# Kernel optimization log

Measured on AMD Instinct MI355X. Metric: run time of the kernel, lower is better.

Reference implementation:

```python
import jax, jax.numpy as jnp
import numpy as np

D_QUERY = 512
D_AUDIO = 512
D_OUT = 512
B, HW, S = 16, 4096, 1024


def setup_inputs() -> dict:
    key = jax.random.key(0)
    ks = jax.random.split(key, 8)
    sc_q = 1.0 / np.sqrt(D_QUERY)
    sc_a = 1.0 / np.sqrt(D_AUDIO)
    return {
        "x": jax.random.normal(ks[0], (B, HW, D_QUERY), dtype=jnp.float32),
        "audio_embed": jax.random.normal(ks[1], (B, S, D_AUDIO), dtype=jnp.float32),
        "Wq": jax.random.uniform(ks[2], (D_QUERY, D_OUT), jnp.float32, -sc_q, sc_q),
        "bq": jax.random.uniform(ks[3], (D_OUT,), jnp.float32, -sc_q, sc_q),
        "Wk": jax.random.uniform(ks[4], (D_AUDIO, D_OUT), jnp.float32, -sc_a, sc_a),
        "bk": jax.random.uniform(ks[5], (D_OUT,), jnp.float32, -sc_a, sc_a),
        "Wv": jax.random.uniform(ks[6], (D_AUDIO, D_OUT), jnp.float32, -sc_a, sc_a),
        "bv": jax.random.uniform(ks[7], (D_OUT,), jnp.float32, -sc_a, sc_a),
    }


def reference(x, audio_embed, Wq, bq, Wk, bk, Wv, bv):
    # Linear projections (nn.Linear: y = x @ W^T + b; we store W already transposed)
    Q = x @ Wq + bq                      # [B, HW, D_OUT]
    K = audio_embed @ Wk + bk            # [B, S, D_OUT]
    V = audio_embed @ Wv + bv            # [B, S, D_OUT]
    scale = 1.0 / (K.shape[-1] ** 0.5)   # divide by sqrt(d_out), per source
    scores = jnp.einsum("bnd,bsd->bns", Q, K) * scale  # [B, HW, S]
    attn = jax.nn.softmax(scores, axis=-1)
    return jnp.einsum("bns,bsd->bnd", attn, V)         # [B, HW, D_OUT]
```

## Files before the change

### kernel.cpp

```cpp
#include <hip/hip_runtime.h>
#include <hip/hip_bf16.h>

typedef __attribute__((ext_vector_type(8))) short bf16x8;
typedef __attribute__((ext_vector_type(4))) float f32x4;
typedef __attribute__((ext_vector_type(4))) unsigned short ushort4v;

#define AS1 __attribute__((address_space(1)))
#define AS3 __attribute__((address_space(3)))

__device__ __forceinline__ float bf_bits_to_f(short s) {
  unsigned int u = ((unsigned int)(unsigned short)s) << 16;
  union { unsigned int u; float f; } c; c.u = u; return c.f;
}
__device__ __forceinline__ unsigned short f_to_bf_bits(float f) {
  union { float f; unsigned int u; } c; c.f = f;
  unsigned int r = c.u + 0x7FFFu + ((c.u >> 16) & 1u);
  return (unsigned short)(r >> 16);
}

__device__ __forceinline__ int fsw(int row) { return ((row >> 1) & 3) << 4; }

__global__ __launch_bounds__(256) void cvt_bf16_kernel(const float* __restrict__ in,
                                                       unsigned short* __restrict__ out,
                                                       long n) {
  const long nchunks = n >> 2;
  const long stride = (long)gridDim.x * 256;
  for (long c = (long)blockIdx.x * 256 + threadIdx.x; c < nchunks; c += stride) {
    f32x4 v = *(const f32x4*)(in + c * 4);
    ushort4v o;
    o[0] = f_to_bf_bits(v[0]); o[1] = f_to_bf_bits(v[1]);
    o[2] = f_to_bf_bits(v[2]); o[3] = f_to_bf_bits(v[3]);
    *(ushort4v*)(out + c * 4) = o;
  }
}

__global__ __launch_bounds__(256) void transpose1_kernel(
    const float* __restrict__ W, unsigned short* __restrict__ T) {
  __shared__ float t[32][33];
  const int tx = threadIdx.x & 31, ty = threadIdx.x >> 5;
  const int n0 = blockIdx.x * 32, k0 = blockIdx.y * 32;
#pragma unroll
  for (int j = 0; j < 4; ++j)
    t[ty + 8 * j][tx] = W[(long)(k0 + ty + 8 * j) * 512 + n0 + tx];
  __syncthreads();
#pragma unroll
  for (int j = 0; j < 4; ++j)
    T[(long)(n0 + ty + 8 * j) * 512 + k0 + tx] = f_to_bf_bits(t[tx][ty + 8 * j]);
}

__global__ __launch_bounds__(256) void wvec_kernel(const float* __restrict__ Wk,
                                                   const float* __restrict__ bq,
                                                   float* __restrict__ w, const float s) {
  const int q = blockIdx.x * 4 + (threadIdx.x >> 6);
  const int lane = threadIdx.x & 63;
  const float* row = Wk + (long)q * 512 + lane * 8;
  const f32x4 a0 = *(const f32x4*)row;
  const f32x4 a1 = *(const f32x4*)(row + 4);
  const f32x4 b0 = *(const f32x4*)(bq + lane * 8);
  const f32x4 b1 = *(const f32x4*)(bq + lane * 8 + 4);
  float d = a0[0]*b0[0] + a0[1]*b0[1] + a0[2]*b0[2] + a0[3]*b0[3]
          + a1[0]*b1[0] + a1[1]*b1[1] + a1[2]*b1[2] + a1[3]*b1[3];
  for (int off = 1; off < 64; off <<= 1) d += __shfl_xor(d, off);
  if (lane == 0) w[q] = d * s;
}

__global__ __launch_bounds__(256) void cvec_kernel(const unsigned short* __restrict__ ab,
                                                   const float* __restrict__ w,
                                                   float* __restrict__ cv) {
  const long row = (long)blockIdx.x * 4 + (threadIdx.x >> 6);
  const int lane = threadIdx.x & 63;
  const bf16x8 a = *(const bf16x8*)(ab + row * 512 + lane * 8);
  const f32x4 w0 = *(const f32x4*)(w + lane * 8);
  const f32x4 w1 = *(const f32x4*)(w + lane * 8 + 4);
  float d = 0.f;
#pragma unroll
  for (int e = 0; e < 4; ++e) d += bf_bits_to_f(a[e]) * w0[e];
#pragma unroll
  for (int e = 0; e < 4; ++e) d += bf_bits_to_f(a[4 + e]) * w1[e];
  for (int off = 1; off < 64; off <<= 1) d += __shfl_xor(d, off);
  if (lane == 0) cv[row] = d;
}

template <bool BIAS, bool TRANSOUT, bool AFP32>
__global__ __launch_bounds__(256) void gemm_kernel(
    const void* __restrict__ Aptr,
    const unsigned short* __restrict__ BT,
    const float* __restrict__ bias,
    unsigned short* __restrict__ Cout,
    const int K, const float scale,
    const long strideA, const long strideBT, const long strideC, const int ldc,
    const int nx, const int ny) {
  __shared__ unsigned short lds[8192];
  const int nwg = gridDim.x;
  const int chunk = nwg >> 3;
  const int bid = blockIdx.x;
  const int swz = (bid & 7) * chunk + (bid >> 3);
  const int bx = swz % nx;
  const int t1 = swz / nx;
  const int by = t1 % ny;
  const int bz = t1 / ny;

  const int tid = threadIdx.x;
  const int lane = tid & 63;
  const int wv = tid >> 6;
  const int wr = wv >> 1, wc = wv & 1;
  const unsigned short* Ab = (const unsigned short*)Aptr + (long)bz * strideA + (long)by * 128 * K;
  const float* Af = (const float*)Aptr + (long)bz * strideA + (long)by * 128 * K;
  const unsigned short* Bb = BT + (long)bz * strideBT + (long)bx * 128 * K;

  f32x4 acc[4][4];
#pragma unroll
  for (int m = 0; m < 4; ++m)
#pragma unroll
    for (int n = 0; n < 4; ++n) acc[m][n] = (f32x4){0.f, 0.f, 0.f, 0.f};

  const int r15 = lane & 15, g = lane >> 4;
  const int kiters = K >> 5;
  const int asw = fsw(r15);

  int arow[2], acs[2];
#pragma unroll
  for (int i = 0; i < 2; ++i) {
    const int c = i * 4 + wv;
    const int boff = c * 1024 + lane * 16;
    arow[i] = boff >> 6;
    acs[i] = (boff & 63) ^ fsw(arow[i]);
  }
  f32x4 pa[2][2];
  if (AFP32) {
#pragma unroll
    for (int i = 0; i < 2; ++i) {
      const float* s = Af + (long)arow[i] * K + (acs[i] >> 1);
      pa[i][0] = *(const f32x4*)s;
      pa[i][1] = *(const f32x4*)(s + 4);
    }
  }

  for (int kt = 0; kt < kiters; ++kt) {
#pragma unroll
    for (int i = 0; i < 2; ++i) {
      const int c = i * 4 + wv;
      const char* srcB = (const char*)Bb + (long)arow[i] * (K * 2) + kt * 64 + acs[i];
      __builtin_amdgcn_global_load_lds(
          (const AS1 void*)srcB, (AS3 void*)(lds + 4096 + c * 512), 16, 0, 0);
      if (!AFP32) {
        const char* srcA = (const char*)Ab + (long)arow[i] * (K * 2) + kt * 64 + acs[i];
        __builtin_amdgcn_global_load_lds(
            (const AS1 void*)srcA, (AS3 void*)(lds + c * 512), 16, 0, 0);
      }
    }
    if (AFP32) {
#pragma unroll
      for (int i = 0; i < 2; ++i) {
        const int c = i * 4 + wv;
        bf16x8 w;
#pragma unroll
        for (int e = 0; e < 4; ++e) {
          w[e] = (short)f_to_bf_bits(pa[i][0][e]);
          w[4 + e] = (short)f_to_bf_bits(pa[i][1][e]);
        }
        *(bf16x8*)&lds[c * 512 + lane * 8] = w;
      }
      if (kt < kiters - 1) {
#pragma unroll
        for (int i = 0; i < 2; ++i) {
          const float* s = Af + (long)arow[i] * K + (kt + 1) * 32 + (acs[i] >> 1);
          pa[i][0] = *(const f32x4*)s;
          pa[i][1] = *(const f32x4*)(s + 4);
        }
      }
    }
    __syncthreads();

    bf16x8 af[4], bf[4];
#pragma unroll
    for (int m = 0; m < 4; ++m)
      af[m] = *(const bf16x8*)((const char*)lds + (wr * 64 + m * 16 + r15) * 64 + (g * 16 ^ asw));
#pragma unroll
    for (int n = 0; n < 4; ++n)
      bf[n] = *(const bf16x8*)((const char*)lds + 8192 +
                               (wc * 64 + n * 16 + r15) * 64 + (g * 16 ^ asw));
#pragma unroll
    for (int m = 0; m < 4; ++m)
#pragma unroll
      for (int n = 0; n < 4; ++n)
        acc[m][n] = __builtin_amdgcn_mfma_f32_16x16x32_bf16(af[m], bf[n], acc[m][n], 0, 0, 0);
    __syncthreads();
  }

  const long crow0 = (long)by * 128 + wr * 64;
  const long ccol0 = (long)bx * 128 + wc * 64;
#pragma unroll
  for (int n = 0; n < 4; ++n) {
    const long col = ccol0 + n * 16 + r15;
    const float bv = BIAS ? bias[col] : 0.f;
#pragma unroll
    for (int m = 0; m < 4; ++m) {
      const f32x4 v = acc[m][n];
#pragma unroll
      for (int j = 0; j < 4; ++j) {
        const long row = crow0 + m * 16 + g * 4 + j;
        const float val = (v[j] + bv) * scale;
        const long idx = TRANSOUT ? (col * (long)ldc + row) : (row * (long)ldc + col);
        (Cout + (long)bz * strideC)[idx] = f_to_bf_bits(val);
      }
    }
  }
}

template <bool EXPSTATS, bool DIVSTATS>
__global__ __launch_bounds__(512, 2) void gemm256_kernel(
    const unsigned short* __restrict__ A,
    const unsigned short* __restrict__ BT,
    void* __restrict__ Cout,
    const int K,
    const long strideA, const long strideBT, const long strideC, const int ldc,
    const int nx, const int ny, float* __restrict__ stats,
    const float* __restrict__ cbias) {
  __shared__ __align__(16) char halfb[4][32768];
  __shared__ float ssum[256][4];
  __shared__ float invl[256];

  const int nwg = gridDim.x;
  const int chunk = nwg >> 3;
  const int bid = blockIdx.x;
  const int swz = (bid & 7) * chunk + (bid >> 3);
  const int bx = swz % nx;
  const int t1 = swz / nx;
  const int by = t1 % ny;
  const int bz = t1 / ny;

  const int tid = threadIdx.x;
  const int lane = tid & 63;
  const int w = tid >> 6;
  const int wm = w >> 2, wn = w & 3;
  const int r15 = lane & 15, g = lane >> 4;
  const int asw = fsw(r15);

  const char* Abyt = (const char*)(A + (long)bz * strideA + (long)by * 256 * K);
  const char* Bbyt = (const char*)(BT + (long)bz * strideBT + (long)bx * 256 * K);
  const long rsb = (long)K * 2;

  if (DIVSTATS) {
    if (tid < 256) {
      const f32x4 s = *(const f32x4*)&stats[((long)bz * 4096 + (long)by * 256 + tid) * 4];
      invl[tid] = 1.f / (s[0] + s[1] + s[2] + s[3]);
    }
  }
  __builtin_amdgcn_sched_barrier(0);

  const int srow0 = tid >> 2;
  const int scol = ((tid & 3) << 4) ^ fsw(srow0);
  const long aoff0 = (long)srow0 * rsb + scol;
  const long aoff1 = (long)(srow0 + 128) * rsb + scol;
  const int dbase = tid * 16;

  auto stage = [&](int s) {
    char* h = halfb[s & 3];
    const long kb = (long)s * 64;
    __builtin_amdgcn_global_load_lds((const AS1 void*)(Abyt + aoff0 + kb),
                                     (AS3 void*)(h + dbase), 16, 0, 0);
    __builtin_amdgcn_global_load_lds((const AS1 void*)(Abyt + aoff1 + kb),
                                     (AS3 void*)(h + 8192 + dbase), 16, 0, 0);
    __builtin_amdgcn_global_load_lds((const AS1 void*)(Bbyt + aoff0 + kb),
                                     (AS3 void*)(h + 16384 + dbase), 16, 0, 0);
    __builtin_amdgcn_global_load_lds((const AS1 void*)(Bbyt + aoff1 + kb),
                                     (AS3 void*)(h + 24576 + dbase), 16, 0, 0);
  };

  f32x4 acc[8][4];
#pragma unroll
  for (int m = 0; m < 8; ++m)
#pragma unroll
    for (int n = 0; n < 4; ++n) acc[m][n] = (f32x4){0.f, 0.f, 0.f, 0.f};

  const int kslices = K >> 5;

  stage(0);
  stage(1);
  stage(2);
  asm volatile("s_waitcnt vmcnt(8)" ::: "memory");
  __builtin_amdgcn_s_barrier();
  __builtin_amdgcn_sched_barrier(0);

  for (int s = 0; s < kslices; ++s) {
    const char* hA = halfb[s & 3];
    const char* hB = halfb[s & 3] + 16384;
    bf16x8 fa[8], fb[4];
#pragma unroll
    for (int m = 0; m < 8; ++m)
      fa[m] = *(const bf16x8*)(hA + (wm * 128 + m * 16 + r15) * 64 + ((g * 16) ^ asw));
#pragma unroll
    for (int n = 0; n < 4; ++n)
      fb[n] = *(const bf16x8*)(hB + (wn * 64 + n * 16 + r15) * 64 + ((g * 16) ^ asw));
    __builtin_amdgcn_sched_barrier(0);
    if (s < kslices - 2) asm volatile("s_waitcnt vmcnt(4)" ::: "memory");
    else                 asm volatile("s_waitcnt vmcnt(0)" ::: "memory");
    __builtin_amdgcn_s_barrier();
    asm volatile("s_waitcnt lgkmcnt(0)" ::: "memory");
    __builtin_amdgcn_sched_barrier(0);
    if (s + 3 < kslices) stage(s + 3);
    __builtin_amdgcn_s_setprio(1);
#pragma unroll
    for (int m = 0; m < 8; ++m)
#pragma unroll
      for (int n = 0; n < 4; ++n)
        acc[m][n] = __builtin_amdgcn_mfma_f32_16x16x32_bf16(fa[m], fb[n], acc[m][n], 0, 0, 0);
    __builtin_amdgcn_s_setprio(0);
    __builtin_amdgcn_sched_barrier(0);
  }

  if (EXPSTATS) {
    float cb[4];
#pragma unroll
    for (int n = 0; n < 4; ++n)
      cb[n] = cbias[(long)bz * 1024 + (long)bx * 256 + wn * 64 + n * 16 + r15];
#pragma unroll
    for (int m = 0; m < 8; ++m)
#pragma unroll
      for (int n = 0; n < 4; ++n)
#pragma unroll
        for (int j = 0; j < 4; ++j) acc[m][n][j] = __expf(acc[m][n][j] + cb[n]);
#pragma unroll
    for (int m = 0; m < 8; ++m)
#pragma unroll
      for (int j = 0; j < 4; ++j) {
        float s = acc[m][0][j] + acc[m][1][j] + acc[m][2][j] + acc[m][3][j];
        s += __shfl_xor(s, 1);
        s += __shfl_xor(s, 2);
        s += __shfl_xor(s, 4);
        s += __shfl_xor(s, 8);
        if (r15 == 0) ssum[wm * 128 + m * 16 + g * 4 + j][wn] = s;
      }
    __syncthreads();
    if (tid < 256) {
      const float t = ssum[tid][0] + ssum[tid][1] + ssum[tid][2] + ssum[tid][3];
      stats[((long)bz * 4096 + (long)by * 256 + tid) * 4 + bx] = t;
    }
  }

  const long crow0 = (long)by * 256 + wm * 128;
  const long ccol0 = (long)bx * 256 + wn * 64;
#pragma unroll
  for (int m = 0; m < 8; ++m)
#pragma unroll
    for (int j = 0; j < 4; ++j) {
      const int rl = wm * 128 + m * 16 + g * 4 + j;
      const long row = crow0 + m * 16 + g * 4 + j;
#pragma unroll
      for (int n = 0; n < 4; ++n) {
        const long col = ccol0 + n * 16 + r15;
        if (EXPSTATS) {
          ((unsigned short*)Cout + (long)bz * strideC)[row * (long)ldc + col] =
              f_to_bf_bits(acc[m][n][j]);
        } else {
          const float sc = DIVSTATS ? invl[rl] : 1.f;
          ((float*)Cout + (long)bz * strideC)[row * (long)ldc + col] = acc[m][n][j] * sc;
        }
      }
    }
}

extern "C" void kernel_launch(void* const* d_in, const int* in_sizes, int n_in,
                              void* d_out, int out_size, void* d_ws, size_t ws_size,
                              hipStream_t stream) {
  (void)in_sizes; (void)n_in; (void)out_size; (void)ws_size;
  const float* x     = (const float*)d_in[0];
  const float* audio = (const float*)d_in[1];
  const float* Wq    = (const float*)d_in[2];
  const float* bq    = (const float*)d_in[3];
  const float* Wk    = (const float*)d_in[4];
  const float* bk    = (const float*)d_in[5];  (void)bk;
  const float* Wv    = (const float*)d_in[6];
  const float* bv    = (const float*)d_in[7];
  float* out = (float*)d_out;

  const float s = 0.044194173824159216f;

  char* ws = (char*)d_ws;
  size_t off = 0;
  auto carve = [&](size_t bytes) { char* p = ws + off; off += (bytes + 255) & ~(size_t)255; return p; };
  unsigned short* xb  = (unsigned short*)carve((size_t)65536 * 512 * 2);
  unsigned short* ab  = (unsigned short*)carve((size_t)16384 * 512 * 2);
  unsigned short* wkb = (unsigned short*)carve((size_t)512 * 512 * 2);
  unsigned short* wvt = (unsigned short*)carve((size_t)512 * 512 * 2);
  unsigned short* G   = (unsigned short*)carve((size_t)512 * 512 * 2);
  unsigned short* KMb = (unsigned short*)carve((size_t)16384 * 512 * 2);
  unsigned short* Vt  = (unsigned short*)carve((size_t)16384 * 512 * 2);
  unsigned short* Pb  = (unsigned short*)carve((size_t)65536 * 1024 * 2);
  float*          ls  = (float*)carve((size_t)65536 * 4 * 4);
  float*          wv_ = (float*)carve((size_t)512 * 4);
  float*          cv  = (float*)carve((size_t)16384 * 4);

  cvt_bf16_kernel<<<2048, 256, 0, stream>>>(x, xb, (long)65536 * 512);
  cvt_bf16_kernel<<<1024, 256, 0, stream>>>(audio, ab, (long)16384 * 512);
  cvt_bf16_kernel<<<256, 256, 0, stream>>>(Wk, wkb, (long)512 * 512);
  transpose1_kernel<<<dim3(16, 16), 256, 0, stream>>>(Wv, wvt);
  gemm_kernel<false, false, true><<<16, 256, 0, stream>>>(
      Wq, wkb, nullptr, G, 512, s, 0, 0, 0, 512, 4, 4);
  wvec_kernel<<<128, 256, 0, stream>>>(Wk, bq, wv_, s);
  cvec_kernel<<<4096, 256, 0, stream>>>(ab, wv_, cv);
  gemm_kernel<true, true, false><<<4 * 8 * 16, 256, 0, stream>>>(
      ab, wvt, bv, Vt, 512, 1.f, (long)1024 * 512, 0, (long)512 * 1024, 1024, 4, 8);
  gemm_kernel<false, false, false><<<4 * 8 * 16, 256, 0, stream>>>(
      ab, G, nullptr, KMb, 512, 1.f, (long)1024 * 512, 0, (long)1024 * 512, 512, 4, 8);
  gemm256_kernel<true, false><<<4 * 16 * 16, 512, 0, stream>>>(
      xb, KMb, Pb, 512,
      (long)4096 * 512, (long)1024 * 512, (long)4096 * 1024, 1024, 4, 16, ls, cv);
  gemm256_kernel<false, true><<<2 * 16 * 16, 512, 0, stream>>>(
      Pb, Vt, out, 1024,
      (long)4096 * 1024, (long)512 * 1024, (long)4096 * 512, 512, 2, 16, ls, nullptr);
}
```

Baseline: 328.5 us.

## Fuse fp32-to-bf16 conversion into GEMM loaders and merge V/K projections

```diff
diff --git a/kernel.cpp b/kernel.cpp
--- a/kernel.cpp
+++ b/kernel.cpp
@@ -64,19 +64,17 @@
   if (lane == 0) w[q] = d * s;
 }
 
-__global__ __launch_bounds__(256) void cvec_kernel(const unsigned short* __restrict__ ab,
+__global__ __launch_bounds__(256) void cvec_kernel(const float* __restrict__ audio,
                                                    const float* __restrict__ w,
                                                    float* __restrict__ cv) {
   const long row = (long)blockIdx.x * 4 + (threadIdx.x >> 6);
   const int lane = threadIdx.x & 63;
-  const bf16x8 a = *(const bf16x8*)(ab + row * 512 + lane * 8);
+  const f32x4 a0 = *(const f32x4*)(audio + row * 512 + lane * 8);
+  const f32x4 a1 = *(const f32x4*)(audio + row * 512 + lane * 8 + 4);
   const f32x4 w0 = *(const f32x4*)(w + lane * 8);
   const f32x4 w1 = *(const f32x4*)(w + lane * 8 + 4);
-  float d = 0.f;
-#pragma unroll
-  for (int e = 0; e < 4; ++e) d += bf_bits_to_f(a[e]) * w0[e];
-#pragma unroll
-  for (int e = 0; e < 4; ++e) d += bf_bits_to_f(a[4 + e]) * w1[e];
+  float d = a0[0]*w0[0] + a0[1]*w0[1] + a0[2]*w0[2] + a0[3]*w0[3]
+          + a1[0]*w1[0] + a1[1]*w1[1] + a1[2]*w1[2] + a1[3]*w1[3];
   for (int off = 1; off < 64; off <<= 1) d += __shfl_xor(d, off);
   if (lane == 0) cv[row] = d;
 }
@@ -208,9 +206,126 @@
   }
 }
 
-template <bool EXPSTATS, bool DIVSTATS>
+__global__ __launch_bounds__(256) void projdual_kernel(
+    const float* __restrict__ audio,
+    const unsigned short* __restrict__ wvt,
+    const unsigned short* __restrict__ G,
+    const float* __restrict__ bv,
+    unsigned short* __restrict__ Vt,
+    unsigned short* __restrict__ KMb) {
+  __shared__ unsigned short lds[8192];
+  const int nwg = gridDim.x;
+  const int chunk = nwg >> 3;
+  const int bid = blockIdx.x;
+  const int swz = (bid & 7) * chunk + (bid >> 3);
+  const int bx = swz & 7;
+  const int t1 = swz >> 3;
+  const int by = t1 & 7;
+  const int bz = t1 >> 3;
+
+  const int tid = threadIdx.x;
+  const int lane = tid & 63;
+  const int wv = tid >> 6;
+  const int wr = wv >> 1, wc = wv & 1;
+  const float* Af = audio + (long)bz * 1024 * 512 + (long)by * 128 * 512;
+  const unsigned short* Bb = (bx < 4) ? (wvt + (long)bx * 128 * 512)
+                                      : (G + (long)(bx - 4) * 128 * 512);
+
+  f32x4 acc[4][4];
+#pragma unroll
+  for (int m = 0; m < 4; ++m)
+#pragma unroll
+    for (int n = 0; n < 4; ++n) acc[m][n] = (f32x4){0.f, 0.f, 0.f, 0.f};
+
+  const int r15 = lane & 15, g = lane >> 4;
+  const int asw = fsw(r15);
+
+  int arow[2], acs[2];
+#pragma unroll
+  for (int i = 0; i < 2; ++i) {
+    const int c = i * 4 + wv;
+    const int boff = c * 1024 + lane * 16;
+    arow[i] = boff >> 6;
+    acs[i] = (boff & 63) ^ fsw(arow[i]);
+  }
+  f32x4 pa[2][2];
+#pragma unroll
+  for (int i = 0; i < 2; ++i) {
+    const float* s = Af + (long)arow[i] * 512 + (acs[i] >> 1);
+    pa[i][0] = *(const f32x4*)s;
+    pa[i][1] = *(const f32x4*)(s + 4);
+  }
+
+  for (int kt = 0; kt < 16; ++kt) {
+#pragma unroll
+    for (int i = 0; i < 2; ++i) {
+      const int c = i * 4 + wv;
+      const char* srcB = (const char*)Bb + (long)arow[i] * 1024 + kt * 64 + acs[i];
+      __builtin_amdgcn_global_load_lds(
+          (const AS1 void*)srcB, (AS3 void*)(lds + 4096 + c * 512), 16, 0, 0);
+    }
+#pragma unroll
+    for (int i = 0; i < 2; ++i) {
+      const int c = i * 4 + wv;
+      bf16x8 w;
+#pragma unroll
+      for (int e = 0; e < 4; ++e) {
+        w[e] = (short)f_to_bf_bits(pa[i][0][e]);
+        w[4 + e] = (short)f_to_bf_bits(pa[i][1][e]);
+      }
+      *(bf16x8*)&lds[c * 512 + lane * 8] = w;
+    }
+    if (kt < 15) {
+#pragma unroll
+      for (int i = 0; i < 2; ++i) {
+        const float* s = Af + (long)arow[i] * 512 + (kt + 1) * 32 + (acs[i] >> 1);
+        pa[i][0] = *(const f32x4*)s;
+        pa[i][1] = *(const f32x4*)(s + 4);
+      }
+    }
+    __syncthreads();
+
+    bf16x8 af[4], bf[4];
+#pragma unroll
+    for (int m = 0; m < 4; ++m)
+      af[m] = *(const bf16x8*)((const char*)lds + (wr * 64 + m * 16 + r15) * 64 + (g * 16 ^ asw));
+#pragma unroll
+    for (int n = 0; n < 4; ++n)
+      bf[n] = *(const bf16x8*)((const char*)lds + 8192 +
+                               (wc * 64 + n * 16 + r15) * 64 + (g * 16 ^ asw));
+#pragma unroll
+    for (int m = 0; m < 4; ++m)
+#pragma unroll
+      for (int n = 0; n < 4; ++n)
+        acc[m][n] = __builtin_amdgcn_mfma_f32_16x16x32_bf16(af[m], bf[n], acc[m][n], 0, 0, 0);
+    __syncthreads();
+  }
+
+  const long crow0 = (long)by * 128 + wr * 64;
+  const long ccol0 = (long)bx * 128 + wc * 64;
+#pragma unroll
+  for (int n = 0; n < 4; ++n) {
+    const long col = ccol0 + n * 16 + r15;
+    const float bvv = (bx < 4) ? bv[col] : 0.f;
+#pragma unroll
+    for (int m = 0; m < 4; ++m) {
+      const f32x4 v = acc[m][n];
+#pragma unroll
+      for (int j = 0; j < 4; ++j) {
+        const long row = crow0 + m * 16 + g * 4 + j;
+        const float val = v[j] + bvv;
+        if (bx < 4)
+          Vt[(long)bz * 512 * 1024 + col * 1024 + row] = f_to_bf_bits(val);
+        else
+          KMb[(long)bz * 1024 * 512 + row * 512 + (col - 512)] = f_to_bf_bits(val);
+      }
+    }
+  }
+}
+
+template <bool EXPSTATS, bool DIVSTATS, bool AFP32>
 __global__ __launch_bounds__(512, 2) void gemm256_kernel(
-    const unsigned short* __restrict__ A,
+    const void* __restrict__ Aptr,
     const unsigned short* __restrict__ BT,
     void* __restrict__ Cout,
     const int K,
@@ -237,7 +352,9 @@
   const int r15 = lane & 15, g = lane >> 4;
   const int asw = fsw(r15);
 
-  const char* Abyt = (const char*)(A + (long)bz * strideA + (long)by * 256 * K);
+  const unsigned short* Abf = (const unsigned short*)Aptr + (long)bz * strideA + (long)by * 256 * K;
+  const float* Afp = (const float*)Aptr + (long)bz * strideA + (long)by * 256 * K;
+  const char* Abyt = (const char*)Abf;
   const char* Bbyt = (const char*)(BT + (long)bz * strideBT + (long)bx * 256 * K);
   const long rsb = (long)K * 2;
 
@@ -254,19 +371,26 @@
   const long aoff0 = (long)srow0 * rsb + scol;
   const long aoff1 = (long)(srow0 + 128) * rsb + scol;
   const int dbase = tid * 16;
-
+  const float* AF0 = Afp + (long)srow0 * K + (scol >> 1);
+  const float* AF1 = Afp + (long)(srow0 + 128) * K + (scol >> 1);
+
+  auto gl = [&](const char* src, char* dst) {
+    __builtin_amdgcn_global_load_lds((const AS1 void*)src, (AS3 void*)dst, 16, 0, 0);
+  };
   auto stage = [&](int s) {
     char* h = halfb[s & 3];
     const long kb = (long)s * 64;
-    __builtin_amdgcn_global_load_lds((const AS1 void*)(Abyt + aoff0 + kb),
-                                     (AS3 void*)(h + dbase), 16, 0, 0);
-    __builtin_amdgcn_global_load_lds((const AS1 void*)(Abyt + aoff1 + kb),
-                                     (AS3 void*)(h + 8192 + dbase), 16, 0, 0);
-    __builtin_amdgcn_global_load_lds((const AS1 void*)(Bbyt + aoff0 + kb),
-                                     (AS3 void*)(h + 16384 + dbase), 16, 0, 0);
-    __builtin_amdgcn_global_load_lds((const AS1 void*)(Bbyt + aoff1 + kb),
-                                     (AS3 void*)(h + 24576 + dbase), 16, 0, 0);
+    gl(Abyt + aoff0 + kb, h + dbase);
+    gl(Abyt + aoff1 + kb, h + 8192 + dbase);
+    gl(Bbyt + aoff0 + kb, h + 16384 + dbase);
+    gl(Bbyt + aoff1 + kb, h + 24576 + dbase);
   };
+  auto stageB = [&](int s) {
+    char* h = halfb[s & 3];
+    const long kb = (long)s * 64;
+    gl(Bbyt + aoff0 + kb, h + 16384 + dbase);
+    gl(Bbyt + aoff1 + kb, h + 24576 + dbase);
+  };
 
   f32x4 acc[8][4];
 #pragma unroll
@@ -275,40 +399,98 @@
     for (int n = 0; n < 4; ++n) acc[m][n] = (f32x4){0.f, 0.f, 0.f, 0.f};
 
   const int kslices = K >> 5;
-
-  stage(0);
-  stage(1);
-  stage(2);
-  asm volatile("s_waitcnt vmcnt(8)" ::: "memory");
-  __builtin_amdgcn_s_barrier();
-  __builtin_amdgcn_sched_barrier(0);
-
-  for (int s = 0; s < kslices; ++s) {
-    const char* hA = halfb[s & 3];
-    const char* hB = halfb[s & 3] + 16384;
-    bf16x8 fa[8], fb[4];
-#pragma unroll
-    for (int m = 0; m < 8; ++m)
-      fa[m] = *(const bf16x8*)(hA + (wm * 128 + m * 16 + r15) * 64 + ((g * 16) ^ asw));
-#pragma unroll
-    for (int n = 0; n < 4; ++n)
-      fb[n] = *(const bf16x8*)(hB + (wn * 64 + n * 16 + r15) * 64 + ((g * 16) ^ asw));
+  f32x4 paE[4], paO[4];
+
+  if (AFP32) {
+    paE[0] = *(const f32x4*)AF0;       paE[1] = *(const f32x4*)(AF0 + 4);
+    paE[2] = *(const f32x4*)AF1;       paE[3] = *(const f32x4*)(AF1 + 4);
+    paO[0] = *(const f32x4*)(AF0 + 32); paO[1] = *(const f32x4*)(AF0 + 36);
+    paO[2] = *(const f32x4*)(AF1 + 32); paO[3] = *(const f32x4*)(AF1 + 36);
+    asm volatile("s_waitcnt vmcnt(0)" ::: "memory");
+#pragma unroll
+    for (int hv = 0; hv < 2; ++hv) {
+      const f32x4* P = hv ? paO : paE;
+      char* h = halfb[hv];
+      bf16x8 w0, w1;
+#pragma unroll
+      for (int e = 0; e < 4; ++e) {
+        w0[e] = (short)f_to_bf_bits(P[0][e]); w0[4 + e] = (short)f_to_bf_bits(P[1][e]);
+        w1[e] = (short)f_to_bf_bits(P[2][e]); w1[4 + e] = (short)f_to_bf_bits(P[3][e]);
+      }
+      *(bf16x8*)(h + dbase) = w0;
+      *(bf16x8*)(h + 8192 + dbase) = w1;
+    }
+    stageB(0); stageB(1); stageB(2);
+    paE[0] = *(const f32x4*)(AF0 + 64); paE[1] = *(const f32x4*)(AF0 + 68);
+    paE[2] = *(const f32x4*)(AF1 + 64); paE[3] = *(const f32x4*)(AF1 + 68);
+    paO[0] = *(const f32x4*)(AF0 + 96); paO[1] = *(const f32x4*)(AF0 + 100);
+    paO[2] = *(const f32x4*)(AF1 + 96); paO[3] = *(const f32x4*)(AF1 + 100);
+    __syncthreads();
+  } else {
+    stage(0); stage(1); stage(2);
+    asm volatile("s_waitcnt vmcnt(8)" ::: "memory");
+    __builtin_amdgcn_s_barrier();
     __builtin_amdgcn_sched_barrier(0);
-    if (s < kslices - 2) asm volatile("s_waitcnt vmcnt(4)" ::: "memory");
-    else                 asm volatile("s_waitcnt vmcnt(0)" ::: "memory");
-    __builtin_amdgcn_s_barrier();
-    asm volatile("s_waitcnt lgkmcnt(0)" ::: "memory");
-    __builtin_amdgcn_sched_barrier(0);
-    if (s + 3 < kslices) stage(s + 3);
-    __builtin_amdgcn_s_setprio(1);
-#pragma unroll
-    for (int m = 0; m < 8; ++m)
-#pragma unroll
-      for (int n = 0; n < 4; ++n)
-        acc[m][n] = __builtin_amdgcn_mfma_f32_16x16x32_bf16(fa[m], fb[n], acc[m][n], 0, 0, 0);
-    __builtin_amdgcn_s_setprio(0);
-    __builtin_amdgcn_sched_barrier(0);
-  }
+  }
+
+#define PHASE(S, PA)                                                                   \
+  {                                                                                    \
+    const int s_ = (S);                                                                \
+    const char* hA = halfb[s_ & 3];                                                    \
+    const char* hB = halfb[s_ & 3] + 16384;                                            \
+    bf16x8 fa[8], fb[4];                                                               \
+    _Pragma("unroll") for (int m = 0; m < 8; ++m)                                      \
+      fa[m] = *(const bf16x8*)(hA + (wm * 128 + m * 16 + r15) * 64 + ((g * 16) ^ asw)); \
+    _Pragma("unroll") for (int n = 0; n < 4; ++n)                                      \
+      fb[n] = *(const bf16x8*)(hB + (wn * 64 + n * 16 + r15) * 64 + ((g * 16) ^ asw)); \
+    __builtin_amdgcn_sched_barrier(0);                                                 \
+    if (AFP32) {                                                                       \
+      if (s_ < kslices - 3)       asm volatile("s_waitcnt vmcnt(6)" ::: "memory");     \
+      else if (s_ == kslices - 3) asm volatile("s_waitcnt vmcnt(2)" ::: "memory");     \
+      else                        asm volatile("s_waitcnt vmcnt(0)" ::: "memory");     \
+    } else {                                                                           \
+      if (s_ < kslices - 2) asm volatile("s_waitcnt vmcnt(4)" ::: "memory");           \
+      else                  asm volatile("s_waitcnt vmcnt(0)" ::: "memory");           \
+    }                                                                                  \
+    asm volatile("s_waitcnt lgkmcnt(0)" ::: "memory");                                 \
+    __builtin_amdgcn_s_barrier();                                                      \
+    __builtin_amdgcn_sched_barrier(0);                                                 \
+    if (AFP32) {                                                                       \
+      if (s_ + 2 < kslices) {                                                          \
+        char* hW = halfb[(s_ + 2) & 3];                                                \
+        bf16x8 w0, w1;                                                                 \
+        _Pragma("unroll") for (int e = 0; e < 4; ++e) {                                \
+          w0[e] = (short)f_to_bf_bits(PA[0][e]);                                       \
+          w0[4 + e] = (short)f_to_bf_bits(PA[1][e]);                                   \
+          w1[e] = (short)f_to_bf_bits(PA[2][e]);                                       \
+          w1[4 + e] = (short)f_to_bf_bits(PA[3][e]);                                   \
+        }                                                                              \
+        *(bf16x8*)(hW + dbase) = w0;                                                   \
+        *(bf16x8*)(hW + 8192 + dbase) = w1;                                            \
+      }                                                                                \
+      if (s_ + 3 < kslices) stageB(s_ + 3);                                            \
+      if (s_ + 4 < kslices) {                                                          \
+        const float* p0 = AF0 + (long)(s_ + 4) * 32;                                   \
+        const float* p1 = AF1 + (long)(s_ + 4) * 32;                                   \
+        PA[0] = *(const f32x4*)p0; PA[1] = *(const f32x4*)(p0 + 4);                    \
+        PA[2] = *(const f32x4*)p1; PA[3] = *(const f32x4*)(p1 + 4);                    \
+      }                                                                                \
+    } else {                                                                           \
+      if (s_ + 3 < kslices) stage(s_ + 3);                                             \
+    }                                                                                  \
+    __builtin_amdgcn_s_setprio(1);                                                     \
+    _Pragma("unroll") for (int m = 0; m < 8; ++m)                                      \
+      _Pragma("unroll") for (int n = 0; n < 4; ++n)                                    \
+        acc[m][n] = __builtin_amdgcn_mfma_f32_16x16x32_bf16(fa[m], fb[n], acc[m][n], 0, 0, 0); \
+    __builtin_amdgcn_s_setprio(0);                                                     \
+    __builtin_amdgcn_sched_barrier(0);                                                 \
+  }
+
+  for (int s = 0; s < kslices; s += 2) {
+    PHASE(s, paE);
+    PHASE(s + 1, paO);
+  }
+#undef PHASE
 
   if (EXPSTATS) {
     float cb[4];
@@ -380,8 +562,6 @@
   char* ws = (char*)d_ws;
   size_t off = 0;
   auto carve = [&](size_t bytes) { char* p = ws + off; off += (bytes + 255) & ~(size_t)255; return p; };
-  unsigned short* xb  = (unsigned short*)carve((size_t)65536 * 512 * 2);
-  unsigned short* ab  = (unsigned short*)carve((size_t)16384 * 512 * 2);
   unsigned short* wkb = (unsigned short*)carve((size_t)512 * 512 * 2);
   unsigned short* wvt = (unsigned short*)carve((size_t)512 * 512 * 2);
   unsigned short* G   = (unsigned short*)carve((size_t)512 * 512 * 2);
@@ -392,22 +572,17 @@
   float*          wv_ = (float*)carve((size_t)512 * 4);
   float*          cv  = (float*)carve((size_t)16384 * 4);
 
-  cvt_bf16_kernel<<<2048, 256, 0, stream>>>(x, xb, (long)65536 * 512);
-  cvt_bf16_kernel<<<1024, 256, 0, stream>>>(audio, ab, (long)16384 * 512);
   cvt_bf16_kernel<<<256, 256, 0, stream>>>(Wk, wkb, (long)512 * 512);
   transpose1_kernel<<<dim3(16, 16), 256, 0, stream>>>(Wv, wvt);
   gemm_kernel<false, false, true><<<16, 256, 0, stream>>>(
       Wq, wkb, nullptr, G, 512, s, 0, 0, 0, 512, 4, 4);
   wvec_kernel<<<128, 256, 0, stream>>>(Wk, bq, wv_, s);
-  cvec_kernel<<<4096, 256, 0, stream>>>(ab, wv_, cv);
-  gemm_kernel<true, true, false><<<4 * 8 * 16, 256, 0, stream>>>(
-      ab, wvt, bv, Vt, 512, 1.f, (long)1024 * 512, 0, (long)512 * 1024, 1024, 4, 8);
-  gemm_kernel<false, false, false><<<4 * 8 * 16, 256, 0, stream>>>(
-      ab, G, nullptr, KMb, 512, 1.f, (long)1024 * 512, 0, (long)1024 * 512, 512, 4, 8);
-  gemm256_kernel<true, false><<<4 * 16 * 16, 512, 0, stream>>>(
-      xb, KMb, Pb, 512,
+  cvec_kernel<<<4096, 256, 0, stream>>>(audio, wv_, cv);
+  projdual_kernel<<<8 * 8 * 16, 256, 0, stream>>>(audio, wvt, G, bv, Vt, KMb);
+  gemm256_kernel<true, false, true><<<4 * 16 * 16, 512, 0, stream>>>(
+      x, KMb, Pb, 512,
       (long)4096 * 512, (long)1024 * 512, (long)4096 * 1024, 1024, 4, 16, ls, cv);
-  gemm256_kernel<false, true><<<2 * 16 * 16, 512, 0, stream>>>(
+  gemm256_kernel<false, true, false><<<2 * 16 * 16, 512, 0, stream>>>(
       Pb, Vt, out, 1024,
       (long)4096 * 1024, (long)512 * 1024, (long)4096 * 512, 512, 2, 16, ls, nullptr);
 }
```

Measured after the change: 327.9 us. Within noise of the previous version (-0.2%).

## Fuse audio bf16 conversion into a single dual V/K projection GEMM

Applied to the files above, without the earlier changes.

```diff
diff --git a/kernel.cpp b/kernel.cpp
--- a/kernel.cpp
+++ b/kernel.cpp
@@ -64,19 +64,17 @@
   if (lane == 0) w[q] = d * s;
 }
 
-__global__ __launch_bounds__(256) void cvec_kernel(const unsigned short* __restrict__ ab,
+__global__ __launch_bounds__(256) void cvec_kernel(const float* __restrict__ audio,
                                                    const float* __restrict__ w,
                                                    float* __restrict__ cv) {
   const long row = (long)blockIdx.x * 4 + (threadIdx.x >> 6);
   const int lane = threadIdx.x & 63;
-  const bf16x8 a = *(const bf16x8*)(ab + row * 512 + lane * 8);
+  const f32x4 a0 = *(const f32x4*)(audio + row * 512 + lane * 8);
+  const f32x4 a1 = *(const f32x4*)(audio + row * 512 + lane * 8 + 4);
   const f32x4 w0 = *(const f32x4*)(w + lane * 8);
   const f32x4 w1 = *(const f32x4*)(w + lane * 8 + 4);
-  float d = 0.f;
-#pragma unroll
-  for (int e = 0; e < 4; ++e) d += bf_bits_to_f(a[e]) * w0[e];
-#pragma unroll
-  for (int e = 0; e < 4; ++e) d += bf_bits_to_f(a[4 + e]) * w1[e];
+  float d = a0[0]*w0[0] + a0[1]*w0[1] + a0[2]*w0[2] + a0[3]*w0[3]
+          + a1[0]*w1[0] + a1[1]*w1[1] + a1[2]*w1[2] + a1[3]*w1[3];
   for (int off = 1; off < 64; off <<= 1) d += __shfl_xor(d, off);
   if (lane == 0) cv[row] = d;
 }
@@ -208,6 +206,123 @@
   }
 }
 
+__global__ __launch_bounds__(256) void projdual_kernel(
+    const float* __restrict__ audio,
+    const unsigned short* __restrict__ wvt,
+    const unsigned short* __restrict__ G,
+    const float* __restrict__ bv,
+    unsigned short* __restrict__ Vt,
+    unsigned short* __restrict__ KMb) {
+  __shared__ unsigned short lds[8192];
+  const int nwg = gridDim.x;
+  const int chunk = nwg >> 3;
+  const int bid = blockIdx.x;
+  const int swz = (bid & 7) * chunk + (bid >> 3);
+  const int bx = swz & 7;
+  const int t1 = swz >> 3;
+  const int by = t1 & 7;
+  const int bz = t1 >> 3;
+
+  const int tid = threadIdx.x;
+  const int lane = tid & 63;
+  const int wv = tid >> 6;
+  const int wr = wv >> 1, wc = wv & 1;
+  const float* Af = audio + (long)bz * 1024 * 512 + (long)by * 128 * 512;
+  const unsigned short* Bb = (bx < 4) ? (wvt + (long)bx * 128 * 512)
+                                      : (G + (long)(bx - 4) * 128 * 512);
+
+  f32x4 acc[4][4];
+#pragma unroll
+  for (int m = 0; m < 4; ++m)
+#pragma unroll
+    for (int n = 0; n < 4; ++n) acc[m][n] = (f32x4){0.f, 0.f, 0.f, 0.f};
+
+  const int r15 = lane & 15, g = lane >> 4;
+  const int asw = fsw(r15);
+
+  int arow[2], acs[2];
+#pragma unroll
+  for (int i = 0; i < 2; ++i) {
+    const int c = i * 4 + wv;
+    const int boff = c * 1024 + lane * 16;
+    arow[i] = boff >> 6;
+    acs[i] = (boff & 63) ^ fsw(arow[i]);
+  }
+  f32x4 pa[2][2];
+#pragma unroll
+  for (int i = 0; i < 2; ++i) {
+    const float* s = Af + (long)arow[i] * 512 + (acs[i] >> 1);
+    pa[i][0] = *(const f32x4*)s;
+    pa[i][1] = *(const f32x4*)(s + 4);
+  }
+
+  for (int kt = 0; kt < 16; ++kt) {
+#pragma unroll
+    for (int i = 0; i < 2; ++i) {
+      const int c = i * 4 + wv;
+      const char* srcB = (const char*)Bb + (long)arow[i] * 1024 + kt * 64 + acs[i];
+      __builtin_amdgcn_global_load_lds(
+          (const AS1 void*)srcB, (AS3 void*)(lds + 4096 + c * 512), 16, 0, 0);
+    }
+#pragma unroll
+    for (int i = 0; i < 2; ++i) {
+      const int c = i * 4 + wv;
+      bf16x8 w;
+#pragma unroll
+      for (int e = 0; e < 4; ++e) {
+        w[e] = (short)f_to_bf_bits(pa[i][0][e]);
+        w[4 + e] = (short)f_to_bf_bits(pa[i][1][e]);
+      }
+      *(bf16x8*)&lds[c * 512 + lane * 8] = w;
+    }
+    if (kt < 15) {
+#pragma unroll
+      for (int i = 0; i < 2; ++i) {
+        const float* s = Af + (long)arow[i] * 512 + (kt + 1) * 32 + (acs[i] >> 1);
+        pa[i][0] = *(const f32x4*)s;
+        pa[i][1] = *(const f32x4*)(s + 4);
+      }
+    }
+    __syncthreads();
+
+    bf16x8 af[4], bf[4];
+#pragma unroll
+    for (int m = 0; m < 4; ++m)
+      af[m] = *(const bf16x8*)((const char*)lds + (wr * 64 + m * 16 + r15) * 64 + (g * 16 ^ asw));
+#pragma unroll
+    for (int n = 0; n < 4; ++n)
+      bf[n] = *(const bf16x8*)((const char*)lds + 8192 +
+                               (wc * 64 + n * 16 + r15) * 64 + (g * 16 ^ asw));
+#pragma unroll
+    for (int m = 0; m < 4; ++m)
+#pragma unroll
+      for (int n = 0; n < 4; ++n)
+        acc[m][n] = __builtin_amdgcn_mfma_f32_16x16x32_bf16(af[m], bf[n], acc[m][n], 0, 0, 0);
+    __syncthreads();
+  }
+
+  const long crow0 = (long)by * 128 + wr * 64;
+  const long ccol0 = (long)bx * 128 + wc * 64;
+#pragma unroll
+  for (int n = 0; n < 4; ++n) {
+    const long col = ccol0 + n * 16 + r15;
+    const float bvv = (bx < 4) ? bv[col] : 0.f;
+#pragma unroll
+    for (int m = 0; m < 4; ++m) {
+      const f32x4 v = acc[m][n];
+#pragma unroll
+      for (int j = 0; j < 4; ++j) {
+        const long row = crow0 + m * 16 + g * 4 + j;
+        const float val = v[j] + bvv;
+        if (bx < 4)
+          Vt[(long)bz * 512 * 1024 + col * 1024 + row] = f_to_bf_bits(val);
+        else
+          KMb[(long)bz * 1024 * 512 + row * 512 + (col - 512)] = f_to_bf_bits(val);
+      }
+    }
+  }
+}
+
 template <bool EXPSTATS, bool DIVSTATS>
 __global__ __launch_bounds__(512, 2) void gemm256_kernel(
     const unsigned short* __restrict__ A,
@@ -381,7 +496,6 @@
   size_t off = 0;
   auto carve = [&](size_t bytes) { char* p = ws + off; off += (bytes + 255) & ~(size_t)255; return p; };
   unsigned short* xb  = (unsigned short*)carve((size_t)65536 * 512 * 2);
-  unsigned short* ab  = (unsigned short*)carve((size_t)16384 * 512 * 2);
   unsigned short* wkb = (unsigned short*)carve((size_t)512 * 512 * 2);
   unsigned short* wvt = (unsigned short*)carve((size_t)512 * 512 * 2);
   unsigned short* G   = (unsigned short*)carve((size_t)512 * 512 * 2);
@@ -393,17 +507,13 @@
   float*          cv  = (float*)carve((size_t)16384 * 4);
 
   cvt_bf16_kernel<<<2048, 256, 0, stream>>>(x, xb, (long)65536 * 512);
-  cvt_bf16_kernel<<<1024, 256, 0, stream>>>(audio, ab, (long)16384 * 512);
   cvt_bf16_kernel<<<256, 256, 0, stream>>>(Wk, wkb, (long)512 * 512);
   transpose1_kernel<<<dim3(16, 16), 256, 0, stream>>>(Wv, wvt);
   gemm_kernel<false, false, true><<<16, 256, 0, stream>>>(
       Wq, wkb, nullptr, G, 512, s, 0, 0, 0, 512, 4, 4);
   wvec_kernel<<<128, 256, 0, stream>>>(Wk, bq, wv_, s);
-  cvec_kernel<<<4096, 256, 0, stream>>>(ab, wv_, cv);
-  gemm_kernel<true, true, false><<<4 * 8 * 16, 256, 0, stream>>>(
-      ab, wvt, bv, Vt, 512, 1.f, (long)1024 * 512, 0, (long)512 * 1024, 1024, 4, 8);
-  gemm_kernel<false, false, false><<<4 * 8 * 16, 256, 0, stream>>>(
-      ab, G, nullptr, KMb, 512, 1.f, (long)1024 * 512, 0, (long)1024 * 512, 512, 4, 8);
+  cvec_kernel<<<4096, 256, 0, stream>>>(audio, wv_, cv);
+  projdual_kernel<<<8 * 8 * 16, 256, 0, stream>>>(audio, wvt, G, bv, Vt, KMb);
   gemm256_kernel<true, false><<<4 * 16 * 16, 512, 0, stream>>>(
       xb, KMb, Pb, 512,
       (long)4096 * 512, (long)1024 * 512, (long)4096 * 1024, 1024, 4, 16, ls, cv);
```

Result: slower. 342.1 us (+4.1%).
